# Kernel optimization log

Measured on AMD Instinct MI355X. Metric: run time of the kernel, lower is better.

Reference implementation:

```python
import jax, jax.numpy as jnp
import numpy as np

# Module configuration (matches init_kwargs)
B = 128           # batch
C = 21            # in_channels
L = 2048          # in_features
W = 32            # window_size
S = 8             # strides
O = 16            # out_channels
EPS = 1e-6
M = int((L - W) / S - EPS)      # number of regularly-strided windows (251)
NW = M + 1                       # total windows incl. clamped last one (252)
NK = O * NW                      # 4032
# window start positions: j*S for j<M, last window clamped to L-W
STARTS = np.concatenate([np.arange(M) * S, np.array([L - W])]).astype(np.int32)


def setup_inputs() -> dict:
    key = jax.random.key(0)
    kx, kw = jax.random.split(key)
    x = jax.random.normal(kx, (B, C, L), dtype=jnp.float32)
    # original init: 2*(rand-0.5)/sqrt(W*C), uniform in [-1,1]/sqrt(W*C)
    weight = (2.0 * (jax.random.uniform(kw, (NK, W * C), dtype=jnp.float32) - 0.5)
              / np.sqrt(W * C).astype(np.float32))
    return {"x": x, "weight": weight}


def reference(x, weight):
    # im2col gather implied by the sparse fbank: patches[b,c,j,w] = x[b,c,starts[j]+w]
    idx = jnp.asarray(STARTS)[:, None] + jnp.arange(W)[None, :]   # (NW, W)
    patches = x[:, :, idx]                                        # (B, C, NW, W)
    # weight rows are n = j*O + o, columns laid out k*W + w (channel-major)
    w4 = weight.reshape(NW, O, C, W)                              # (NW, O, C, W)
    # h[b, j*O+o] = sum_{c,w} patches[b,c,j,w] * w4[j,o,c,w]
    h = jnp.einsum('bcjw,jocw->bjo', patches, w4)                 # (B, NW, O)
    return h.reshape(B, NK)
```

## Files before the change

kernel.cpp:

```cpp
#include <hip/hip_runtime.h>
#include <hip/hip_bf16.h>

#define Bb   128
#define Cc   21
#define Ll   2048
#define Ss   8
#define Oo   16
#define NWw  252
#define NKk  4032
#define Kk   672
#define KP   680

typedef __attribute__((ext_vector_type(8))) short  short8;
typedef __attribute__((ext_vector_type(4))) float  f32x4;

static __device__ __forceinline__ unsigned short f2bf(float f) {
    union { __hip_bfloat16 h; unsigned short u; } cv;
    cv.h = __float2bfloat16(f);
    return cv.u;
}

static __device__ __forceinline__ short8 cvt8(const float4 a0, const float4 a1) {
    short8 a;
    a[0] = (short)f2bf(a0.x); a[1] = (short)f2bf(a0.y);
    a[2] = (short)f2bf(a0.z); a[3] = (short)f2bf(a0.w);
    a[4] = (short)f2bf(a1.x); a[5] = (short)f2bf(a1.y);
    a[6] = (short)f2bf(a1.z); a[7] = (short)f2bf(a1.w);
    return a;
}

__global__ __launch_bounds__(512)
void fb_fwd(const float* __restrict__ x, const float* __restrict__ w,
            float* __restrict__ out) {
    __shared__ unsigned short ws[Oo * KP];

    const int bid = blockIdx.x;
    const int j   = (bid & 7) * 32 + (bid >> 3);
    if (j >= NWw) return;
    const int s    = (j < NWw - 1) ? j * Ss : (Ll - 32);
    const int tid  = threadIdx.x;
    const int lane = tid & 63;
    const int wv   = tid >> 6;
    const int col  = lane & 15;
    const int quad = lane >> 4;

    const float* xrow = x + ((size_t)(wv * 16 + col) * Cc) * Ll + s + quad * 8;
    float4 a0[Cc], a1[Cc];
#pragma unroll
    for (int c = 0; c < Cc; ++c) {
        a0[c] = *(const float4*)(xrow + (size_t)c * Ll);
        a1[c] = *(const float4*)(xrow + (size_t)c * Ll + 4);
    }

    {
        const f32x4* wj4 = (const f32x4*)(w + (size_t)j * Oo * Kk);
        for (int t = tid; t < Oo * (Kk / 4); t += 512) {
            f32x4 v = __builtin_nontemporal_load(wj4 + t);
            int o = t / (Kk / 4);
            int r = t - o * (Kk / 4);
            *(ushort4*)&ws[o * KP + r * 4] =
                make_ushort4(f2bf(v[0]), f2bf(v[1]), f2bf(v[2]), f2bf(v[3]));
        }
    }

    short8 afr[Cc];
#pragma unroll
    for (int c = 0; c < Cc; ++c) afr[c] = cvt8(a0[c], a1[c]);

    __syncthreads();

    const unsigned short* wrow = &ws[col * KP + quad * 8];
    f32x4 acc = {0.f, 0.f, 0.f, 0.f};
#pragma unroll
    for (int c = 0; c < Cc; ++c)
        acc = __builtin_amdgcn_mfma_f32_16x16x32_bf16(
            afr[c], *(const short8*)(wrow + c * 32), acc, 0, 0, 0);

    const int rbase = wv * 16 + quad * 4;
    float* op = out + (size_t)rbase * NKk + j * 16 + col;
#pragma unroll
    for (int r = 0; r < 4; ++r)
        __builtin_nontemporal_store(acc[r], &op[(size_t)r * NKk]);
}

extern "C" void kernel_launch(void* const* d_in, const int* in_sizes, int n_in,
                              void* d_out, int out_size, void* d_ws, size_t ws_size,
                              hipStream_t stream) {
    const float* x = (const float*)d_in[0];
    const float* w = (const float*)d_in[1];
    float* out = (float*)d_out;
    fb_fwd<<<dim3(256), dim3(512), 0, stream>>>(x, w, out);
}
```

Measured before the change: 85.14 us.

## Group four windows per block and split batch into quarters

Each block now handles four consecutive windows for a 32-row batch quarter instead of one window for all 128 rows. The block stages the four windows' weights (about 43 KB of fp32) into LDS as bf16. Weight loads are issued up front into registers in two halves so they overlap with the x loads and conversion. This reorganises the work split and adds latency hiding for the weight staging. The cost is that each weight slice is now reloaded by four blocks (once per batch quarter), and the larger LDS footprint and register buffers may lower occupancy.

```diff
diff --git a/kernel.cpp b/kernel.cpp
--- a/kernel.cpp
+++ b/kernel.cpp
@@ -32,19 +32,31 @@
 __global__ __launch_bounds__(512)
 void fb_fwd(const float* __restrict__ x, const float* __restrict__ w,
             float* __restrict__ out) {
-    __shared__ unsigned short ws[Oo * KP];
+    __shared__ unsigned short ws[4 * Oo * KP];
 
     const int bid = blockIdx.x;
-    const int j   = (bid & 7) * 32 + (bid >> 3);
-    if (j >= NWw) return;
-    const int s    = (j < NWw - 1) ? j * Ss : (Ll - 32);
+    const int r   = bid & 7;
+    const int idx = bid >> 3;
+    const int g   = r * 8 + (idx >> 2);
+    if (g > 62) return;
+    const int bq   = idx & 3;
     const int tid  = threadIdx.x;
     const int lane = tid & 63;
     const int wv   = tid >> 6;
+    const int wm   = wv >> 2;
+    const int ww   = wv & 3;
     const int col  = lane & 15;
     const int quad = lane >> 4;
+    const int j    = g * 4 + ww;
+    const int s_loc = (j < NWw - 1) ? ww * 8 : 32;
 
-    const float* xrow = x + ((size_t)(wv * 16 + col) * Cc) * Ll + s + quad * 8;
+    const f32x4* wj4 = (const f32x4*)w + (size_t)g * 10752;
+    f32x4 wb[21];
+#pragma unroll
+    for (int p = 0; p < 11; ++p) wb[p] = wj4[tid + p * 512];
+
+    const int b = bq * 32 + wm * 16 + col;
+    const float* xrow = x + ((size_t)b * Cc) * Ll + g * 32 + s_loc + quad * 8;
     float4 a0[Cc], a1[Cc];
 #pragma unroll
     for (int c = 0; c < Cc; ++c) {
@@ -52,35 +64,47 @@
         a1[c] = *(const float4*)(xrow + (size_t)c * Ll + 4);
     }
 
-    {
-        const f32x4* wj4 = (const f32x4*)(w + (size_t)j * Oo * Kk);
-        for (int t = tid; t < Oo * (Kk / 4); t += 512) {
-            f32x4 v = __builtin_nontemporal_load(wj4 + t);
-            int o = t / (Kk / 4);
-            int r = t - o * (Kk / 4);
-            *(ushort4*)&ws[o * KP + r * 4] =
-                make_ushort4(f2bf(v[0]), f2bf(v[1]), f2bf(v[2]), f2bf(v[3]));
-        }
+#pragma unroll
+    for (int p = 0; p < 11; ++p) {
+        int t  = tid + p * 512;
+        int oa = t / 168;
+        int r4 = t - oa * 168;
+        *(ushort4*)&ws[oa * KP + r4 * 4] =
+            make_ushort4(f2bf(wb[p][0]), f2bf(wb[p][1]),
+                         f2bf(wb[p][2]), f2bf(wb[p][3]));
     }
+
+#pragma unroll
+    for (int p = 11; p < 21; ++p) wb[p] = wj4[tid + p * 512];
 
     short8 afr[Cc];
 #pragma unroll
     for (int c = 0; c < Cc; ++c) afr[c] = cvt8(a0[c], a1[c]);
 
+#pragma unroll
+    for (int p = 11; p < 21; ++p) {
+        int t  = tid + p * 512;
+        int oa = t / 168;
+        int r4 = t - oa * 168;
+        *(ushort4*)&ws[oa * KP + r4 * 4] =
+            make_ushort4(f2bf(wb[p][0]), f2bf(wb[p][1]),
+                         f2bf(wb[p][2]), f2bf(wb[p][3]));
+    }
+
     __syncthreads();
 
-    const unsigned short* wrow = &ws[col * KP + quad * 8];
+    const unsigned short* wrow = &ws[(ww * Oo + col) * KP + quad * 8];
     f32x4 acc = {0.f, 0.f, 0.f, 0.f};
 #pragma unroll
     for (int c = 0; c < Cc; ++c)
         acc = __builtin_amdgcn_mfma_f32_16x16x32_bf16(
             afr[c], *(const short8*)(wrow + c * 32), acc, 0, 0, 0);
 
-    const int rbase = wv * 16 + quad * 4;
+    const int rbase = bq * 32 + wm * 16 + quad * 4;
     float* op = out + (size_t)rbase * NKk + j * 16 + col;
 #pragma unroll
-    for (int r = 0; r < 4; ++r)
-        __builtin_nontemporal_store(acc[r], &op[(size_t)r * NKk]);
+    for (int rr = 0; rr < 4; ++rr)
+        __builtin_nontemporal_store(acc[rr], &op[(size_t)rr * NKk]);
 }
 
 extern "C" void kernel_launch(void* const* d_in, const int* in_sizes, int n_in,
```

Result: faster. 81.38 us (-4.4%).

## Split channel reduction across two waves per tile with LDS combine, use 1024 threads

Applied to the files above, without the earlier changes.

Doubles the block to 1024 threads and splits each 16-row tile's 21-channel reduction between two waves (10 and 11 channels), combining partial accumulators through shared memory before the store. Weight loads are issued up front into registers before the x loads so they overlap, and the bf16 conversion of x is done per MFMA instead of all at once. This is meant to raise memory-level parallelism and cut per-thread register pressure and latency, at the cost of an extra barrier and LDS round-trip for the reduction.

```diff
diff --git a/kernel.cpp b/kernel.cpp
--- a/kernel.cpp
+++ b/kernel.cpp
@@ -1,7 +1,6 @@
 #include <hip/hip_runtime.h>
 #include <hip/hip_bf16.h>
 
-#define Bb   128
 #define Cc   21
 #define Ll   2048
 #define Ss   8
@@ -29,10 +28,11 @@
     return a;
 }
 
-__global__ __launch_bounds__(512)
+__global__ __launch_bounds__(1024, 4)
 void fb_fwd(const float* __restrict__ x, const float* __restrict__ w,
             float* __restrict__ out) {
     __shared__ unsigned short ws[Oo * KP];
+    __shared__ float rs[8][64][4];
 
     const int bid = blockIdx.x;
     const int j   = (bid & 7) * 32 + (bid >> 3);
@@ -41,46 +41,71 @@
     const int tid  = threadIdx.x;
     const int lane = tid & 63;
     const int wv   = tid >> 6;
+    const int mt   = wv >> 1;
+    const int kh   = wv & 1;
     const int col  = lane & 15;
     const int quad = lane >> 4;
 
-    const float* xrow = x + ((size_t)(wv * 16 + col) * Cc) * Ll + s + quad * 8;
-    float4 a0[Cc], a1[Cc];
+    const f32x4* wj4 = (const f32x4*)(w + (size_t)j * Oo * Kk);
+    const bool has3 = tid < (Oo * (Kk / 4) - 2 * 1024);
+    f32x4 wb0 = wj4[tid];
+    f32x4 wb1 = wj4[tid + 1024];
+    f32x4 wb2;
+    if (has3) wb2 = wj4[tid + 2048];
+
+    const int row   = mt * 16 + col;
+    const int cbase = kh * 10;
+    const float* xrow = x + ((size_t)row * Cc + cbase) * Ll + s + quad * 8;
+    float4 a0[11], a1[11];
 #pragma unroll
-    for (int c = 0; c < Cc; ++c) {
+    for (int c = 0; c < 10; ++c) {
         a0[c] = *(const float4*)(xrow + (size_t)c * Ll);
         a1[c] = *(const float4*)(xrow + (size_t)c * Ll + 4);
     }
+    if (kh) {
+        a0[10] = *(const float4*)(xrow + (size_t)10 * Ll);
+        a1[10] = *(const float4*)(xrow + (size_t)10 * Ll + 4);
+    }
 
     {
-        const f32x4* wj4 = (const f32x4*)(w + (size_t)j * Oo * Kk);
-        for (int t = tid; t < Oo * (Kk / 4); t += 512) {
-            f32x4 v = __builtin_nontemporal_load(wj4 + t);
-            int o = t / (Kk / 4);
-            int r = t - o * (Kk / 4);
-            *(ushort4*)&ws[o * KP + r * 4] =
-                make_ushort4(f2bf(v[0]), f2bf(v[1]), f2bf(v[2]), f2bf(v[3]));
+        int t = tid;         int oa = t / 168; int r4 = t - oa * 168;
+        *(ushort4*)&ws[oa * KP + r4 * 4] =
+            make_ushort4(f2bf(wb0[0]), f2bf(wb0[1]), f2bf(wb0[2]), f2bf(wb0[3]));
+        t = tid + 1024;      oa = t / 168;     r4 = t - oa * 168;
+        *(ushort4*)&ws[oa * KP + r4 * 4] =
+            make_ushort4(f2bf(wb1[0]), f2bf(wb1[1]), f2bf(wb1[2]), f2bf(wb1[3]));
+        if (has3) {
+            t = tid + 2048;  oa = t / 168;     r4 = t - oa * 168;
+            *(ushort4*)&ws[oa * KP + r4 * 4] =
+                make_ushort4(f2bf(wb2[0]), f2bf(wb2[1]), f2bf(wb2[2]), f2bf(wb2[3]));
         }
     }
-
-    short8 afr[Cc];
-#pragma unroll
-    for (int c = 0; c < Cc; ++c) afr[c] = cvt8(a0[c], a1[c]);
-
     __syncthreads();
 
-    const unsigned short* wrow = &ws[col * KP + quad * 8];
+    const unsigned short* wrow = &ws[col * KP + quad * 8 + cbase * 32];
     f32x4 acc = {0.f, 0.f, 0.f, 0.f};
 #pragma unroll
-    for (int c = 0; c < Cc; ++c)
+    for (int c = 0; c < 10; ++c) {
+        short8 afr = cvt8(a0[c], a1[c]);
         acc = __builtin_amdgcn_mfma_f32_16x16x32_bf16(
-            afr[c], *(const short8*)(wrow + c * 32), acc, 0, 0, 0);
+            afr, *(const short8*)(wrow + c * 32), acc, 0, 0, 0);
+    }
+    if (kh) {
+        short8 afr = cvt8(a0[10], a1[10]);
+        acc = __builtin_amdgcn_mfma_f32_16x16x32_bf16(
+            afr, *(const short8*)(wrow + 10 * 32), acc, 0, 0, 0);
+    }
 
-    const int rbase = wv * 16 + quad * 4;
-    float* op = out + (size_t)rbase * NKk + j * 16 + col;
+    if (kh) *(f32x4*)rs[mt][lane] = acc;
+    __syncthreads();
+    if (!kh) {
+        const f32x4 other = *(const f32x4*)rs[mt][lane];
+        const int rbase = mt * 16 + quad * 4;
+        float* op = out + (size_t)rbase * NKk + j * 16 + col;
 #pragma unroll
-    for (int r = 0; r < 4; ++r)
-        __builtin_nontemporal_store(acc[r], &op[(size_t)r * NKk]);
+        for (int rr = 0; rr < 4; ++rr)
+            __builtin_nontemporal_store(acc[rr] + other[rr], &op[(size_t)rr * NKk]);
+    }
 }
 
 extern "C" void kernel_launch(void* const* d_in, const int* in_sizes, int n_in,
@@ -89,5 +114,5 @@
     const float* x = (const float*)d_in[0];
     const float* w = (const float*)d_in[1];
     float* out = (float*)d_out;
-    fb_fwd<<<dim3(256), dim3(512), 0, stream>>>(x, w, out);
+    fb_fwd<<<dim3(256), dim3(1024), 0, stream>>>(x, w, out);
 }
```

After: 81.57 us. 4.2% less time.
